# Kernel optimization log

Measured on AMD Instinct MI355X. Metric: run time of the kernel, lower is better.

The kernel has to match this reference:

```python
import jax, jax.numpy as jnp
import numpy as np

EPS = 1e-05
NUM_HEADS = 8
NUM_GROUPS = 32  # min(32, 512 // 4)


def setup_inputs() -> dict:
    key = jax.random.key(0)
    ks = jax.random.split(key, 5)
    B, C, T, X = 4, 512, 16, 2048
    return {
        "x": jax.random.normal(ks[0], (B, C, T, X), dtype=jnp.float32),
        "gn_w": jnp.ones((C,), dtype=jnp.float32),
        "gn_b": jnp.zeros((C,), dtype=jnp.float32),
        "qkv_w": jax.random.normal(ks[1], (3 * C, C), dtype=jnp.float32) * 0.02,
        "qkv_b": jax.random.normal(ks[2], (3 * C,), dtype=jnp.float32) * 0.02,
        "proj_w": jax.random.normal(ks[3], (C, C), dtype=jnp.float32) * 1e-5,
        "proj_b": jnp.zeros((C,), dtype=jnp.float32),
        "pos_emb": jax.random.normal(ks[4], (NUM_HEADS, 2 * T), dtype=jnp.float32) * 1e-5,
    }


def _group_norm(x, w, b):
    B, C, T, X = x.shape
    g = NUM_GROUPS
    xg = x.reshape(B, g, C // g, T, X)
    mu = xg.mean(axis=(2, 3, 4), keepdims=True)
    var = ((xg - mu) ** 2).mean(axis=(2, 3, 4), keepdims=True)
    xn = ((xg - mu) * jax.lax.rsqrt(var + EPS)).reshape(B, C, T, X)
    return xn * w[None, :, None, None] + b[None, :, None, None]


def reference(x, gn_w, gn_b, qkv_w, qkv_b, proj_w, proj_b, pos_emb):
    dtype = x.dtype
    x = x.astype(jnp.float32)
    B, C, T, X = x.shape
    H = NUM_HEADS
    hc = C // H

    xn = _group_norm(x, gn_w, gn_b)
    # 1x1 conv == channel matmul: [B, 3C, T, X]
    qkv = jnp.einsum('oc,bctx->botx', qkv_w, xn) + qkv_b[None, :, None, None]
    # 'b (n heads c) t x -> n (b x) heads t c'
    qkv = qkv.reshape(B, 3, H, hc, T, X)
    qkv = qkv.transpose(1, 0, 5, 2, 4, 3).reshape(3, B * X, H, T, hc)
    q, k, v = qkv[0], qkv[1], qkv[2]

    scale = 1.0 / np.sqrt(hc)
    attn = jnp.einsum('bhqc,bhkc->bhqk', q, k * scale)  # [(B X), H, T, T]

    i = jnp.arange(T)
    pairwise = i[:, None] - i[None, :] + T - 1        # [T, T] in [0, 2T-2]
    rel = pos_emb[:, pairwise]                         # [H, T, T]

    w = jax.nn.softmax(attn + rel[None], axis=-1)
    out = jnp.einsum('bhqk,bhkc->bhcq', w, v)          # [(B X), H, hc, T]
    # '(b x) h c t -> b (h c) t x'
    out = out.reshape(B, X, H, hc, T).transpose(0, 2, 3, 4, 1).reshape(B, C, T, X)

    y = jnp.einsum('oc,bctx->botx', proj_w, out) + proj_b[None, :, None, None]
    return y.astype(dtype)
```

## Files before the change

### kernel.cpp

```cpp
#include <hip/hip_runtime.h>
#include <math.h>

#define EPSV 1e-5f

typedef _Float16 f16;
typedef _Float16 f16x8 __attribute__((ext_vector_type(8)));
typedef _Float16 f16x4 __attribute__((ext_vector_type(4)));
typedef float f32x4 __attribute__((ext_vector_type(4)));

static constexpr int GROUP_N = 16 * 16 * 2048;

__global__ __launch_bounds__(256) void k_gn_part(const float* __restrict__ x,
                                                 float* __restrict__ psum,
                                                 float* __restrict__ psq) {
    const int blk = blockIdx.x;
    const int tid = threadIdx.x;
    const float* p = x + (size_t)blk * 32768;
    float s = 0.f, q = 0.f;
#pragma unroll
    for (int i = 0; i < 32; ++i) {
        float4 v = *(const float4*)(p + (size_t)(i * 256 + tid) * 4);
        s += v.x + v.y + v.z + v.w;
        q += v.x * v.x + v.y * v.y + v.z * v.z + v.w * v.w;
    }
#pragma unroll
    for (int off = 32; off > 0; off >>= 1) {
        s += __shfl_down(s, off);
        q += __shfl_down(q, off);
    }
    __shared__ float ls[4], lq[4];
    const int wave = tid >> 6, lane = tid & 63;
    if (lane == 0) { ls[wave] = s; lq[wave] = q; }
    __syncthreads();
    if (tid == 0) {
        psum[blk] = ls[0] + ls[1] + ls[2] + ls[3];
        psq[blk]  = lq[0] + lq[1] + lq[2] + lq[3];
    }
}

__global__ void k_gn_final(const float* __restrict__ psum, const float* __restrict__ psq,
                           float* __restrict__ mu, float* __restrict__ rs) {
    const int t = threadIdx.x;
    float s = 0.f, q = 0.f;
#pragma unroll
    for (int i = 0; i < 16; ++i) { s += psum[t * 16 + i]; q += psq[t * 16 + i]; }
    const float m = s / (float)GROUP_N;
    float v = q / (float)GROUP_N - m * m;
    mu[t] = m;
    rs[t] = 1.0f / sqrtf(v + EPSV);
}

__global__ __launch_bounds__(256) void k_fold_sc(const float* __restrict__ gn_w,
                                                 const float* __restrict__ gn_b,
                                                 const float* __restrict__ mu,
                                                 const float* __restrict__ rs,
                                                 float* __restrict__ sc,
                                                 float* __restrict__ beta) {
    const int u = blockIdx.x * 256 + threadIdx.x;
    const int b = u >> 9, c = u & 511;
    const int g = c >> 4;
    const float r = rs[b * 32 + g], m = mu[b * 32 + g];
    const float s = r * gn_w[c];
    sc[u]   = s;
    beta[u] = gn_b[c] - m * s;
}

__global__ __launch_bounds__(256) void k_fold_bias(const float* __restrict__ qkv_w,
                                                   const float* __restrict__ qkv_b,
                                                   const float* __restrict__ beta,
                                                   float* __restrict__ qbias) {
    const int u = blockIdx.x * 256 + threadIdx.x;
    const int b = u / 1536, o = u % 1536;
    float acc = qkv_b[o];
    const float* wr = qkv_w + (size_t)o * 512;
    const float* be = beta + b * 512;
#pragma unroll 4
    for (int c = 0; c < 512; c += 4) {
        float4 w4 = *(const float4*)(wr + c);
        float4 b4 = *(const float4*)(be + c);
        acc += w4.x * b4.x + w4.y * b4.y + w4.z * b4.z + w4.w * b4.w;
    }
    if (o >= 512 && o < 1024) acc *= 0.125f;
    qbias[u] = acc;
}


__global__ __launch_bounds__(256) void k_prep_w(const float* __restrict__ qkv_w,
                                                const float* __restrict__ proj_w,
                                                f16* __restrict__ w16,
                                                f16* __restrict__ p16) {
    const int id = blockIdx.x * 256 + threadIdx.x;
    if (id < 196608) {
        const int e0 = id * 4;
        const int o  = e0 >> 9;
        const float ksc = (o >= 512 && o < 1024) ? 0.125f : 1.0f;
        float4 v = *(const float4*)(qkv_w + e0);
        f16x4 h = { (f16)(v.x * ksc), (f16)(v.y * ksc), (f16)(v.z * ksc), (f16)(v.w * ksc) };
        *(f16x4*)(w16 + e0) = h;
    } else {
        const int e0 = (id - 196608) * 4;
        float4 v = *(const float4*)(proj_w + e0);
        f16x4 h = { (f16)v.x, (f16)v.y, (f16)v.z, (f16)v.w };
        *(f16x4*)(p16 + e0) = h;
    }
}

__global__ __launch_bounds__(256) void k_xt(const float* __restrict__ x,
                                            const float* __restrict__ sc,
                                            const float* __restrict__ beta,
                                            f16* __restrict__ xT) {
    const int x0 = blockIdx.x * 64;
    const int c0 = blockIdx.y * 64;
    const int b  = blockIdx.z >> 4, t = blockIdx.z & 15;
    const int tid = threadIdx.x;
    __shared__ float tile[64][68];
#pragma unroll
    for (int it = 0; it < 4; ++it) {
        int idx = it * 256 + tid;
        int c = idx >> 4, xq = idx & 15;
        int cg = c0 + c;
        float s = sc[b * 512 + cg], be = beta[b * 512 + cg];
        float4 v = *(const float4*)(x + (((size_t)(b * 512 + cg) * 16 + t) * 2048) + x0 + xq * 4);
        tile[c][xq * 4 + 0] = v.x * s + be;
        tile[c][xq * 4 + 1] = v.y * s + be;
        tile[c][xq * 4 + 2] = v.z * s + be;
        tile[c][xq * 4 + 3] = v.w * s + be;
    }
    __syncthreads();
#pragma unroll
    for (int it = 0; it < 2; ++it) {
        int idx = it * 256 + tid;
        int xr = idx >> 3, ch = idx & 7;
        f16x8 h;
#pragma unroll
        for (int e = 0; e < 8; ++e) h[e] = (f16)tile[ch * 8 + e][xr];
        *(f16x8*)(xT + (((size_t)(b * 2048 + x0 + xr) * 16 + t) * 512) + c0 + ch * 8) = h;
    }
}

__global__ __launch_bounds__(256) void k3_mfma(const f16* __restrict__ xT,
                                               const f16* __restrict__ w16,
                                               const float* __restrict__ qkv_b,
                                               const float* __restrict__ pos_emb,
                                               float* __restrict__ out) {
    const int h  = blockIdx.x;
    const int x0 = blockIdx.y * 8;
    const int b  = blockIdx.z;
    const int tid = threadIdx.x;
    const int lane = tid & 63, w = tid >> 6;
    const int wm = w >> 1, wn = w & 1;
    const int t_l = lane & 15, g = lane >> 4;

    __shared__ __attribute__((aligned(16))) char smem[66304];
    f16* a_s = (f16*)smem;
    f16* b_s = (f16*)(smem + 24576);
    float* bias_s = (float*)(smem + 65536);

    if (tid < 192) {
        int gr = tid >> 6;
        bias_s[tid] = qkv_b[gr * 512 + h * 64 + (tid & 63)] * (gr == 1 ? 0.125f : 1.0f);
    }

    f32x4 acc[6][4];
#pragma unroll
    for (int mi = 0; mi < 6; ++mi)
#pragma unroll
        for (int ni = 0; ni < 4; ++ni) acc[mi][ni] = (f32x4){0.f, 0.f, 0.f, 0.f};

    const size_t xT_base = ((size_t)b * 2048 + x0) * 16 * 512;

    for (int ko = 0; ko < 512; ko += 64) {
        __syncthreads();
#pragma unroll
        for (int it = 0; it < 6; ++it) {
            int s = it * 256 + tid;
            int m = s >> 3, ch = s & 7;
            int o = (m >> 6) * 512 + h * 64 + (m & 63);
            uint4 v = *(const uint4*)(w16 + (size_t)o * 512 + ko + ch * 8);
            *(uint4*)(a_s + m * 64 + ((ch ^ (m & 7)) * 8)) = v;
        }
#pragma unroll
        for (int it = 0; it < 4; ++it) {
            int s = it * 256 + tid;
            int n = s >> 3, ch = s & 7;
            uint4 v = *(const uint4*)(xT + xT_base + (size_t)n * 512 + ko + ch * 8);
            *(uint4*)(b_s + n * 64 + ((ch ^ (n & 7)) * 8)) = v;
        }
        __syncthreads();
#pragma unroll
        for (int kk = 0; kk < 2; ++kk) {
            const int kb = kk * 4 + g;
            f16x8 af[6], bf[4];
#pragma unroll
            for (int mi = 0; mi < 6; ++mi) {
                int m = wm * 96 + mi * 16 + t_l;
                af[mi] = *(const f16x8*)(a_s + m * 64 + ((kb ^ (m & 7)) * 8));
            }
#pragma unroll
            for (int ni = 0; ni < 4; ++ni) {
                int n = wn * 64 + ni * 16 + t_l;
                bf[ni] = *(const f16x8*)(b_s + n * 64 + ((kb ^ (n & 7)) * 8));
            }
#pragma unroll
            for (int mi = 0; mi < 6; ++mi)
#pragma unroll
                for (int ni = 0; ni < 4; ++ni)
                    acc[mi][ni] = __builtin_amdgcn_mfma_f32_16x16x32_f16(af[mi], bf[ni], acc[mi][ni], 0, 0, 0);
        }
    }
    __syncthreads();
#pragma unroll
    for (int mi = 0; mi < 6; ++mi)
#pragma unroll
        for (int ni = 0; ni < 4; ++ni) {
            int n  = wn * 64 + ni * 16 + t_l;
            int mb = wm * 96 + mi * 16 + g * 4;
            int byte_off = n * 512 + (((mb >> 6) * 8 + (((mb >> 3) & 7) ^ (n & 7))) * 16) + (mb & 7) * 2;
            f16x4 hv;
#pragma unroll
            for (int r = 0; r < 4; ++r) hv[r] = (f16)(acc[mi][ni][r] + bias_s[mb + r]);
            *(f16x4*)(smem + byte_off) = hv;
        }
    __syncthreads();

#pragma unroll
    for (int xc = 0; xc < 2; ++xc) {
        const int xx = w * 2 + xc;
        const int nb = xx * 16;
        const int nrow = nb + t_l;
        const int rbase = nrow * 512;
        const int sw = nrow & 7;

        f32x4 s_acc = {0.f, 0.f, 0.f, 0.f};
#pragma unroll
        for (int half = 0; half < 2; ++half) {
            int qiA = (g + 4 * half) & 7;
            f16x8 afr = *(const f16x8*)(smem + rbase + ((8 + (qiA ^ sw)) * 16));
            f16x8 bfr = *(const f16x8*)(smem + rbase + ((qiA ^ sw) * 16));
            s_acc = __builtin_amdgcn_mfma_f32_16x16x32_f16(afr, bfr, s_acc, 0, 0, 0);
        }
        float sv[4];
#pragma unroll
        for (int r = 0; r < 4; ++r)
            sv[r] = s_acc[r] + pos_emb[h * 32 + t_l - (g * 4 + r) + 15];
        float mx = fmaxf(fmaxf(sv[0], sv[1]), fmaxf(sv[2], sv[3]));
        mx = fmaxf(mx, __shfl_xor(mx, 16));
        mx = fmaxf(mx, __shfl_xor(mx, 32));
        float es[4], ssum = 0.f;
#pragma unroll
        for (int r = 0; r < 4; ++r) { es[r] = __expf(sv[r] - mx); ssum += es[r]; }
        ssum += __shfl_xor(ssum, 16);
        ssum += __shfl_xor(ssum, 32);
        const float inv = 1.0f / ssum;
        f16x4 pfrag;
#pragma unroll
        for (int r = 0; r < 4; ++r) pfrag[r] = (f16)(es[r] * inv);

        f32x4 o_acc[4];
#pragma unroll
        for (int cb = 0; cb < 4; ++cb) {
            int mV = 128 + cb * 16 + t_l;
            int qiV = (mV >> 3) & 7;
            f16x4 vfrag;
#pragma unroll
            for (int j = 0; j < 4; ++j) {
                int nV = nb + g * 4 + j;
                vfrag[j] = *(const f16*)(smem + nV * 512 + ((16 + (qiV ^ (nV & 7))) * 16) + (mV & 7) * 2);
            }
            f32x4 z = {0.f, 0.f, 0.f, 0.f};
            o_acc[cb] = __builtin_amdgcn_mfma_f32_16x16x16f16(vfrag, pfrag, z, 0, 0, 0);
        }
#pragma unroll
        for (int cb = 0; cb < 4; ++cb) {
            int q = cb * 4 + g;
            int byte_off = rbase + (((q >> 3) * 8 + ((q & 7) ^ sw)) * 16);
            *(f32x4*)(smem + byte_off) = o_acc[cb];
        }
    }
    __syncthreads();

    const int c = tid & 63, tq = tid >> 6;
    const int q = c >> 2;
#pragma unroll
    for (int ti = 0; ti < 4; ++ti) {
        int t = tq * 4 + ti;
        float vals[8];
#pragma unroll
        for (int xx = 0; xx < 8; ++xx) {
            int n2 = xx * 16 + t;
            vals[xx] = *(const float*)(smem + n2 * 512 + (((q >> 3) * 8 + ((q & 7) ^ (n2 & 7))) * 16) + (c & 3) * 4);
        }
        float4 lo = {vals[0], vals[1], vals[2], vals[3]};
        float4 hi = {vals[4], vals[5], vals[6], vals[7]};
        size_t oaddr = (((size_t)b * 512 + h * 64 + c) * 16 + t) * 2048 + x0;
        *(float4*)(out + oaddr) = lo;
        *(float4*)(out + oaddr + 4) = hi;
    }
}

__global__ __launch_bounds__(256) void k4_mfma(const f16* __restrict__ p16,
                                               const float* __restrict__ pb,
                                               float* __restrict__ io) {
    const int x0 = blockIdx.x * 64;
    const int t  = blockIdx.y;
    const int b  = blockIdx.z;
    const int tid = threadIdx.x, lane = tid & 63, w = tid >> 6;

    __shared__ __attribute__((aligned(16))) char smem4[81920];
    f16* in_sT = (f16*)smem4;
    f16* bp_s  = (f16*)(smem4 + 65536);

    const size_t base_in = (((size_t)b * 512) * 16 + t) * 2048 + x0;
#pragma unroll
    for (int it = 0; it < 32; ++it) {
        int s = it * 256 + tid;
        int c = s >> 4, xq = s & 15;
        float4 v = *(const float4*)(io + base_in + (size_t)c * 16 * 2048 + xq * 4);
        int kc = c >> 3, j = c & 7;
        float vv[4] = {v.x, v.y, v.z, v.w};
#pragma unroll
        for (int e = 0; e < 4; ++e) {
            int xx = xq * 4 + e;
            in_sT[xx * 512 + ((kc ^ (xx & 7)) * 8) + j] = (f16)vv[e];
        }
    }

    for (int no = 0; no < 4; ++no) {
        const int o_base = no * 128;
        f32x4 acc[4][2];
#pragma unroll
        for (int mi = 0; mi < 4; ++mi)
#pragma unroll
            for (int nj = 0; nj < 2; ++nj) acc[mi][nj] = (f32x4){0.f, 0.f, 0.f, 0.f};

        for (int ko = 0; ko < 8; ++ko) {
            __syncthreads();
#pragma unroll
            for (int it = 0; it < 4; ++it) {
                int s = it * 256 + tid;
                int orow = s >> 3, ch = s & 7;
                uint4 v = *(const uint4*)(p16 + (size_t)(o_base + orow) * 512 + ko * 64 + ch * 8);
                *(uint4*)(bp_s + orow * 64 + ((ch ^ (orow & 7)) * 8)) = v;
            }
            __syncthreads();
#pragma unroll
            for (int kk = 0; kk < 2; ++kk) {
                const int kb4 = kk * 4 + (lane >> 4);
                f16x8 af[4], bf[2];
#pragma unroll
                for (int mi = 0; mi < 4; ++mi) {
                    int xx = mi * 16 + (lane & 15);
                    int kc = ko * 8 + kb4;
                    af[mi] = *(const f16x8*)(in_sT + xx * 512 + ((kc ^ (xx & 7)) * 8));
                }
#pragma unroll
                for (int nj = 0; nj < 2; ++nj) {
                    int orow = w * 32 + nj * 16 + (lane & 15);
                    bf[nj] = *(const f16x8*)(bp_s + orow * 64 + ((kb4 ^ (orow & 7)) * 8));
                }
#pragma unroll
                for (int mi = 0; mi < 4; ++mi)
#pragma unroll
                    for (int nj = 0; nj < 2; ++nj)
                        acc[mi][nj] = __builtin_amdgcn_mfma_f32_16x16x32_f16(af[mi], bf[nj], acc[mi][nj], 0, 0, 0);
            }
        }
#pragma unroll
        for (int mi = 0; mi < 4; ++mi)
#pragma unroll
            for (int nj = 0; nj < 2; ++nj) {
                int o = o_base + w * 32 + nj * 16 + (lane & 15);
                int xxb = mi * 16 + (lane >> 4) * 4;
                float bias = pb[o];
                float4 ov = {acc[mi][nj][0] + bias, acc[mi][nj][1] + bias,
                             acc[mi][nj][2] + bias, acc[mi][nj][3] + bias};
                *(float4*)(io + (((size_t)b * 512 + o) * 16 + t) * 2048 + x0 + xxb) = ov;
            }
    }
}


__global__ __launch_bounds__(256) void k_qkv_attn(const float* __restrict__ x,
                                                  const float* __restrict__ qkv_w,
                                                  const float* __restrict__ sc,
                                                  const float* __restrict__ qbias,
                                                  const float* __restrict__ pos_emb,
                                                  float* __restrict__ out) {
    const int h  = blockIdx.x;
    const int x0 = blockIdx.y * 4;
    const int b  = blockIdx.z;
    const int tid = threadIdx.x;

    __shared__ float a_s[192][68];
    __shared__ float b_s[64][68];
    __shared__ float w_s[4][16][17];

    const int ty = tid >> 3;
    const int tx = tid & 7;

    float acc[6][8];
#pragma unroll
    for (int j = 0; j < 6; ++j)
#pragma unroll
        for (int k = 0; k < 8; ++k) acc[j][k] = 0.f;

    for (int ko = 0; ko < 512; ko += 64) {
        __syncthreads();
#pragma unroll
        for (int it = 0; it < 12; ++it) {
            int idx = it * 256 + tid;
            int m = idx >> 4;
            int c4 = (idx & 15) * 4;
            int g = m >> 6, i = m & 63;
            int o = g * 512 + h * 64 + i;
            float4 w4 = *(const float4*)(qkv_w + (size_t)o * 512 + ko + c4);
            float4 s4 = *(const float4*)(sc + b * 512 + ko + c4);
            float ksc = (g == 1) ? 0.125f : 1.0f;
            float4 v;
            v.x = w4.x * s4.x * ksc; v.y = w4.y * s4.y * ksc;
            v.z = w4.z * s4.z * ksc; v.w = w4.w * s4.w * ksc;
            *(float4*)&a_s[m][c4] = v;
        }
#pragma unroll
        for (int it = 0; it < 4; ++it) {
            int idx = it * 256 + tid;
            int cc = idx >> 4, t = idx & 15;
            float4 v = *(const float4*)(x + ((size_t)((b * 512 + ko + cc) * 16 + t)) * 2048 + x0);
            *(float4*)&b_s[cc][t * 4] = v;
        }
        __syncthreads();
#pragma unroll 4
        for (int cc = 0; cc < 64; ++cc) {
            float av[6];
#pragma unroll
            for (int j = 0; j < 6; ++j) av[j] = a_s[ty * 6 + j][cc];
            float4 b0 = *(const float4*)&b_s[cc][tx * 8];
            float4 b1 = *(const float4*)&b_s[cc][tx * 8 + 4];
            float bv[8] = {b0.x, b0.y, b0.z, b0.w, b1.x, b1.y, b1.z, b1.w};
#pragma unroll
            for (int j = 0; j < 6; ++j)
#pragma unroll
                for (int k = 0; k < 8; ++k)
                    acc[j][k] = fmaf(av[j], bv[k], acc[j][k]);
        }
    }
#pragma unroll
    for (int j = 0; j < 6; ++j) {
        int m = ty * 6 + j;
        int o = (m >> 6) * 512 + h * 64 + (m & 63);
        float qb = qbias[b * 1536 + o];
#pragma unroll
        for (int k = 0; k < 8; ++k) acc[j][k] += qb;
    }
    __syncthreads();
#pragma unroll
    for (int j = 0; j < 6; ++j)
#pragma unroll
        for (int k = 0; k < 8; ++k)
            a_s[ty * 6 + j][tx * 8 + k] = acc[j][k];
    __syncthreads();

    {
        const int xx = tid >> 6;
        const int t  = (tid >> 2) & 15;
        const int uq = tid & 3;
        float l[4] = {0.f, 0.f, 0.f, 0.f};
        for (int i = 0; i < 64; ++i) {
            float qv = a_s[i][t * 4 + xx];
#pragma unroll
            for (int uu = 0; uu < 4; ++uu)
                l[uu] = fmaf(qv, a_s[64 + i][(uq * 4 + uu) * 4 + xx], l[uu]);
        }
#pragma unroll
        for (int uu = 0; uu < 4; ++uu) {
            int u = uq * 4 + uu;
            w_s[xx][t][u] = l[uu] + pos_emb[h * 32 + t - u + 15];
        }
    }
    __syncthreads();
    if (tid < 64) {
        const int xx = tid >> 4, t = tid & 15;
        float mx = -3.4e38f;
#pragma unroll
        for (int u = 0; u < 16; ++u) mx = fmaxf(mx, w_s[xx][t][u]);
        float ssum = 0.f;
#pragma unroll
        for (int u = 0; u < 16; ++u) {
            float e = __expf(w_s[xx][t][u] - mx);
            w_s[xx][t][u] = e;
            ssum += e;
        }
        float inv = 1.0f / ssum;
#pragma unroll
        for (int u = 0; u < 16; ++u) w_s[xx][t][u] *= inv;
    }
    __syncthreads();
    {
        const int i  = tid & 63;
        const int t4 = tid >> 6;
        float4 varr[16];
#pragma unroll
        for (int u = 0; u < 16; ++u) varr[u] = *(const float4*)&a_s[128 + i][u * 4];
#pragma unroll
        for (int tt = 0; tt < 4; ++tt) {
            int t = t4 * 4 + tt;
            float4 o4 = {0.f, 0.f, 0.f, 0.f};
#pragma unroll
            for (int u = 0; u < 16; ++u) {
                o4.x = fmaf(w_s[0][t][u], varr[u].x, o4.x);
                o4.y = fmaf(w_s[1][t][u], varr[u].y, o4.y);
                o4.z = fmaf(w_s[2][t][u], varr[u].z, o4.z);
                o4.w = fmaf(w_s[3][t][u], varr[u].w, o4.w);
            }
            *(float4*)(out + ((size_t)((b * 512 + h * 64 + i) * 16 + t)) * 2048 + x0) = o4;
        }
    }
}

__global__ __launch_bounds__(256) void k_proj(const float* __restrict__ pw,
                                              const float* __restrict__ pb,
                                              float* __restrict__ io) {
    const int n0 = blockIdx.x * 32;
    const int b  = blockIdx.y;
    const int tid = threadIdx.x;
    __shared__ float in_s[512][36];
    __shared__ float w_s[128][65];

    {
        const float* src = io + (size_t)b * 512 * 32768 + n0;
#pragma unroll
        for (int it = 0; it < 64; ++it) {
            int idx = it * 256 + tid;
            int r = idx >> 5, j = idx & 31;
            in_s[r][j] = src[(size_t)r * 32768 + j];
        }
    }
    __syncthreads();

    const int ty = tid >> 3;
    const int tx = tid & 7;

    for (int mo = 0; mo < 512; mo += 128) {
        float acc[4][4];
#pragma unroll
        for (int j = 0; j < 4; ++j)
#pragma unroll
            for (int k = 0; k < 4; ++k) acc[j][k] = 0.f;

        for (int ko = 0; ko < 512; ko += 64) {
#pragma unroll
            for (int it = 0; it < 32; ++it) {
                int idx = it * 256 + tid;
                int m = idx >> 6, cc = idx & 63;
                w_s[m][cc] = pw[(size_t)(mo + m) * 512 + ko + cc];
            }
            __syncthreads();
#pragma unroll 4
            for (int cc = 0; cc < 64; ++cc) {
                float4 bv = *(const float4*)&in_s[ko + cc][tx * 4];
                float a0 = w_s[ty * 4 + 0][cc];
                float a1 = w_s[ty * 4 + 1][cc];
                float a2 = w_s[ty * 4 + 2][cc];
                float a3 = w_s[ty * 4 + 3][cc];
                acc[0][0] = fmaf(a0, bv.x, acc[0][0]); acc[0][1] = fmaf(a0, bv.y, acc[0][1]);
                acc[0][2] = fmaf(a0, bv.z, acc[0][2]); acc[0][3] = fmaf(a0, bv.w, acc[0][3]);
                acc[1][0] = fmaf(a1, bv.x, acc[1][0]); acc[1][1] = fmaf(a1, bv.y, acc[1][1]);
                acc[1][2] = fmaf(a1, bv.z, acc[1][2]); acc[1][3] = fmaf(a1, bv.w, acc[1][3]);
                acc[2][0] = fmaf(a2, bv.x, acc[2][0]); acc[2][1] = fmaf(a2, bv.y, acc[2][1]);
                acc[2][2] = fmaf(a2, bv.z, acc[2][2]); acc[2][3] = fmaf(a2, bv.w, acc[2][3]);
                acc[3][0] = fmaf(a3, bv.x, acc[3][0]); acc[3][1] = fmaf(a3, bv.y, acc[3][1]);
                acc[3][2] = fmaf(a3, bv.z, acc[3][2]); acc[3][3] = fmaf(a3, bv.w, acc[3][3]);
            }
            __syncthreads();
        }
#pragma unroll
        for (int j = 0; j < 4; ++j) {
            int m = mo + ty * 4 + j;
            float bias = pb[m];
            float4 o4 = {acc[j][0] + bias, acc[j][1] + bias, acc[j][2] + bias, acc[j][3] + bias};
            *(float4*)(io + (size_t)(b * 512 + m) * 32768 + n0 + tx * 4) = o4;
        }
    }
}

extern "C" void kernel_launch(void* const* d_in, const int* in_sizes, int n_in,
                              void* d_out, int out_size, void* d_ws, size_t ws_size,
                              hipStream_t stream) {
    (void)in_sizes; (void)n_in; (void)out_size;
    const float* x       = (const float*)d_in[0];
    const float* gn_w    = (const float*)d_in[1];
    const float* gn_b    = (const float*)d_in[2];
    const float* qkv_w   = (const float*)d_in[3];
    const float* qkv_b   = (const float*)d_in[4];
    const float* proj_w  = (const float*)d_in[5];
    const float* proj_b  = (const float*)d_in[6];
    const float* pos_emb = (const float*)d_in[7];
    float* out = (float*)d_out;

    float* ws    = (float*)d_ws;
    float* psum  = ws;
    float* psq   = ws + 2048;
    float* mu    = ws + 4096;
    float* rs    = ws + 4224;
    float* sc    = ws + 4352;
    float* beta  = ws + 6400;
    float* qbias = ws + 8448;

    const size_t W16_OFF = 65536;
    const size_t P16_OFF = W16_OFF + (size_t)1536 * 512 * 2;
    const size_t XT_OFF  = P16_OFF + (size_t)512 * 512 * 2;
    const size_t NEEDED  = XT_OFF + (size_t)4 * 2048 * 16 * 512 * 2;

    k_gn_part<<<dim3(2048), dim3(256), 0, stream>>>(x, psum, psq);
    k_gn_final<<<dim3(1), dim3(128), 0, stream>>>(psum, psq, mu, rs);
    k_fold_sc<<<dim3(8), dim3(256), 0, stream>>>(gn_w, gn_b, mu, rs, sc, beta);

    if (ws_size >= NEEDED) {
        f16* w16 = (f16*)((char*)d_ws + W16_OFF);
        f16* p16 = (f16*)((char*)d_ws + P16_OFF);
        f16* xT  = (f16*)((char*)d_ws + XT_OFF);
        k_prep_w<<<dim3(1024), dim3(256), 0, stream>>>(qkv_w, proj_w, w16, p16);
        k_xt<<<dim3(32, 8, 64), dim3(256), 0, stream>>>(x, sc, beta, xT);
        k3_mfma<<<dim3(8, 256, 4), dim3(256), 0, stream>>>(xT, w16, qkv_b, pos_emb, out);
        k4_mfma<<<dim3(32, 16, 4), dim3(256), 0, stream>>>(p16, proj_b, out);
    } else {
        k_fold_bias<<<dim3(24), dim3(256), 0, stream>>>(qkv_w, qkv_b, beta, qbias);
        k_qkv_attn<<<dim3(8, 512, 4), dim3(256), 0, stream>>>(x, qkv_w, sc, qbias, pos_emb, out);
        k_proj<<<dim3(1024, 4), dim3(256), 0, stream>>>(proj_w, proj_b, out);
    }
}
```

Baseline: 689.4 us.

## Register-prefetch next K tile in QKV MFMA kernel and remap blocks per XCD

The QKV+attention MFMA kernel now loads the next K slice of weights and activations into registers while MFMAs run on the current shared-memory tile, then stores it after a barrier. This hides global load latency behind compute. The grid is flattened to 1D and remapped so the eight heads of one spatial tile land on the same XCD, which should improve L2 reuse of the xT tile. Launch bounds now request 2 blocks per SM, and address offsets are precomputed. The cost is extra register pressure from the prefetch buffers, which could cause spills.

```diff
diff --git a/kernel.cpp b/kernel.cpp
--- a/kernel.cpp
+++ b/kernel.cpp
@@ -138,14 +138,18 @@
     }
 }
 
-__global__ __launch_bounds__(256) void k3_mfma(const f16* __restrict__ xT,
-                                               const f16* __restrict__ w16,
-                                               const float* __restrict__ qkv_b,
-                                               const float* __restrict__ pos_emb,
-                                               float* __restrict__ out) {
-    const int h  = blockIdx.x;
-    const int x0 = blockIdx.y * 8;
-    const int b  = blockIdx.z;
+__global__ __launch_bounds__(256, 2) void k3_mfma(const f16* __restrict__ xT,
+                                                  const f16* __restrict__ w16,
+                                                  const float* __restrict__ qkv_b,
+                                                  const float* __restrict__ pos_emb,
+                                                  float* __restrict__ out) {
+    const int gid = blockIdx.x;
+    const int xcd = gid & 7, kk_id = gid >> 3;
+    const int h = kk_id & 7;
+    const int p = xcd * 128 + (kk_id >> 3);
+    const int b = p >> 8;
+    const int x0 = (p & 255) * 8;
+
     const int tid = threadIdx.x;
     const int lane = tid & 63, w = tid >> 6;
     const int wm = w >> 1, wn = w & 1;
@@ -161,6 +165,24 @@
         bias_s[tid] = qkv_b[gr * 512 + h * 64 + (tid & 63)] * (gr == 1 ? 0.125f : 1.0f);
     }
 
+    int aoff_g[6], aoff_l[6];
+#pragma unroll
+    for (int it = 0; it < 6; ++it) {
+        int s = it * 256 + tid;
+        int m = s >> 3, ch = s & 7;
+        int o = (m >> 6) * 512 + h * 64 + (m & 63);
+        aoff_g[it] = o * 512 + ch * 8;
+        aoff_l[it] = m * 64 + ((ch ^ (m & 7)) * 8);
+    }
+    int boff_g[4], boff_l[4];
+#pragma unroll
+    for (int it = 0; it < 4; ++it) {
+        int s = it * 256 + tid;
+        int n = s >> 3, ch = s & 7;
+        boff_g[it] = n * 512 + ch * 8;
+        boff_l[it] = n * 64 + ((ch ^ (n & 7)) * 8);
+    }
+
     f32x4 acc[6][4];
 #pragma unroll
     for (int mi = 0; mi < 6; ++mi)
@@ -168,25 +190,27 @@
         for (int ni = 0; ni < 4; ++ni) acc[mi][ni] = (f32x4){0.f, 0.f, 0.f, 0.f};
 
     const size_t xT_base = ((size_t)b * 2048 + x0) * 16 * 512;
-
-    for (int ko = 0; ko < 512; ko += 64) {
-        __syncthreads();
-#pragma unroll
-        for (int it = 0; it < 6; ++it) {
-            int s = it * 256 + tid;
-            int m = s >> 3, ch = s & 7;
-            int o = (m >> 6) * 512 + h * 64 + (m & 63);
-            uint4 v = *(const uint4*)(w16 + (size_t)o * 512 + ko + ch * 8);
-            *(uint4*)(a_s + m * 64 + ((ch ^ (m & 7)) * 8)) = v;
-        }
-#pragma unroll
-        for (int it = 0; it < 4; ++it) {
-            int s = it * 256 + tid;
-            int n = s >> 3, ch = s & 7;
-            uint4 v = *(const uint4*)(xT + xT_base + (size_t)n * 512 + ko + ch * 8);
-            *(uint4*)(b_s + n * 64 + ((ch ^ (n & 7)) * 8)) = v;
-        }
-        __syncthreads();
+    const f16* xTb = xT + xT_base;
+
+    uint4 ra[6], rb[4];
+#pragma unroll
+    for (int i = 0; i < 6; ++i) ra[i] = *(const uint4*)(w16 + aoff_g[i]);
+#pragma unroll
+    for (int i = 0; i < 4; ++i) rb[i] = *(const uint4*)(xTb + boff_g[i]);
+#pragma unroll
+    for (int i = 0; i < 6; ++i) *(uint4*)(a_s + aoff_l[i]) = ra[i];
+#pragma unroll
+    for (int i = 0; i < 4; ++i) *(uint4*)(b_s + boff_l[i]) = rb[i];
+    __syncthreads();
+
+    for (int ko = 64; ko <= 512; ko += 64) {
+        const bool has_next = (ko < 512);
+        if (has_next) {
+#pragma unroll
+            for (int i = 0; i < 6; ++i) ra[i] = *(const uint4*)(w16 + aoff_g[i] + ko);
+#pragma unroll
+            for (int i = 0; i < 4; ++i) rb[i] = *(const uint4*)(xTb + boff_g[i] + ko);
+        }
 #pragma unroll
         for (int kk = 0; kk < 2; ++kk) {
             const int kb = kk * 4 + g;
@@ -206,6 +230,14 @@
 #pragma unroll
                 for (int ni = 0; ni < 4; ++ni)
                     acc[mi][ni] = __builtin_amdgcn_mfma_f32_16x16x32_f16(af[mi], bf[ni], acc[mi][ni], 0, 0, 0);
+        }
+        if (has_next) {
+            __syncthreads();
+#pragma unroll
+            for (int i = 0; i < 6; ++i) *(uint4*)(a_s + aoff_l[i]) = ra[i];
+#pragma unroll
+            for (int i = 0; i < 4; ++i) *(uint4*)(b_s + boff_l[i]) = rb[i];
+            __syncthreads();
         }
     }
     __syncthreads();
@@ -621,7 +653,7 @@
         f16* xT  = (f16*)((char*)d_ws + XT_OFF);
         k_prep_w<<<dim3(1024), dim3(256), 0, stream>>>(qkv_w, proj_w, w16, p16);
         k_xt<<<dim3(32, 8, 64), dim3(256), 0, stream>>>(x, sc, beta, xT);
-        k3_mfma<<<dim3(8, 256, 4), dim3(256), 0, stream>>>(xT, w16, qkv_b, pos_emb, out);
+        k3_mfma<<<dim3(8192), dim3(256), 0, stream>>>(xT, w16, qkv_b, pos_emb, out);
         k4_mfma<<<dim3(32, 16, 4), dim3(256), 0, stream>>>(p16, proj_b, out);
     } else {
         k_fold_bias<<<dim3(24), dim3(256), 0, stream>>>(qkv_w, qkv_b, beta, qbias);
```

After: 1.282 ms. +86.0%, slower.
